# Kernel optimization log

Hardware: AMD Instinct MI355X
Metric: run time of the kernel (lower is better)

Reference implementation:

```python
import jax, jax.numpy as jnp
import numpy as np

B, S, N, C = 8, 256, 256, 64
NH = 8
H, W = 256, 256
D = N * C // NH  # per-head channel dim = 2048
EPS = 1e-12


def window_reverse(windows, ws, Hh, Ww, Cc):
    # windows: (B, S, N, C) -> (B, H*W, C)
    b = windows.shape[0]
    x = windows.reshape(b, Hh // ws[0], Ww // ws[1], ws[0], ws[1], Cc)
    x = x.transpose(0, 1, 3, 2, 4, 5).reshape(b, Hh, Ww, Cc).reshape(b, Hh * Ww, Cc)
    return x


def window_partition(x, ws):
    # x: (B, H, W, C) -> (B, nWin, winElems, C)
    b, hh, ww, cc = x.shape
    x = x.reshape(b, hh // ws[0], ws[0], ww // ws[1], ws[1], cc)
    return x.transpose(0, 1, 3, 2, 4, 5).reshape(b, (hh // ws[0]) * (ww // ws[1]), ws[0] * ws[1], cc)


def setup_inputs() -> dict:
    key = jax.random.key(0)
    ks = jax.random.split(key, 6)
    x = jax.random.normal(ks[0], (B, S, N, C), dtype=jnp.float32)
    qkv_w = jax.random.normal(ks[1], (4 * C, C), dtype=jnp.float32) * 0.02
    qkv_b = jnp.zeros((4 * C,), dtype=jnp.float32)
    proj_w = jax.random.normal(ks[2], (C, C), dtype=jnp.float32) * 0.02
    proj_b = jnp.zeros((C,), dtype=jnp.float32)
    temperature1 = jnp.ones((NH, 1, 1), dtype=jnp.float32)
    temperature2 = jnp.ones((NH, 1, 1), dtype=jnp.float32)
    return {"x": x, "qkv_w": qkv_w, "qkv_b": qkv_b, "proj_w": proj_w,
            "proj_b": proj_b, "temperature1": temperature1, "temperature2": temperature2}


def reference(x, qkv_w, qkv_b, proj_w, proj_b, temperature1, temperature2):
    b, s, n, c = x.shape
    xf = x.reshape(b, s * n, c)
    # fused 4-way qkv projection (q, k, v_H, v_V)
    qkvv = (xf @ qkv_w.T + qkv_b).reshape(b, s, 4, NH, D).transpose(2, 0, 3, 1, 4)
    q, k, v_H, v_V = qkvv[0], qkvv[1], qkvv[2], qkvv[3]  # each (B, NH, S, D)

    # reorient v_V from H-windows (columns) to V-windows (rows)
    v_V = v_V.transpose(0, 2, 1, 3).reshape(b, s, n, c)       # (B,S,N,C)
    v_V = v_V.transpose(0, 2, 1, 3)                           # (B,N,S,C)
    v_V = window_reverse(v_V, (H, 1), H, W, c).reshape(b, H, W, c)
    v_V = window_partition(v_V, (1, W))                       # (B,H,W,C)
    v_V = v_V.transpose(0, 2, 1, 3)                           # (B,W,H,C) == (B,S,N,C)
    v_V = v_V.reshape(b, s, NH, D).transpose(0, 2, 1, 3)      # (B,NH,S,D)

    # cosine attention over S with per-head temperature
    qn = q / jnp.maximum(jnp.linalg.norm(q, axis=-1, keepdims=True), EPS)
    kn = k / jnp.maximum(jnp.linalg.norm(k, axis=-1, keepdims=True), EPS)
    sim = jnp.einsum('bhsd,bhtd->bhst', qn, kn)  # (B,NH,S,S)
    attn_H = jax.nn.softmax(sim * temperature1, axis=-1)
    attn_V = jax.nn.softmax(sim * temperature2, axis=-1)

    x_H = jnp.einsum('bhst,bhtd->bhsd', attn_H, v_H).transpose(0, 2, 1, 3).reshape(b, s * n, c)
    x_V = jnp.einsum('bhst,bhtd->bhsd', attn_V, v_V).transpose(0, 2, 1, 3).reshape(b, s * n, c)

    out = (x_H + x_V) @ proj_w.T + proj_b
    return out.reshape(b, s, n, c)
```

## Files before the change

kernel.cpp:

```cpp
#include <hip/hip_runtime.h>


using half_t = _Float16;
using half8 = __attribute__((ext_vector_type(8))) _Float16;
using f32x4 = __attribute__((ext_vector_type(4))) float;

#define NTOK 524288

#define GLDS(g, l) __builtin_amdgcn_global_load_lds( \
    (const __attribute__((address_space(1))) void*)(g), \
    (__attribute__((address_space(3))) void*)(l), 16, 0, 0)

#define WS_Q      0
#define WS_K      67108864
#define WS_VH     134217728
#define WS_VV     201326592
#define WS_NQ     335544320
#define WS_NK     335609856
#define WS_WH     335675392
#define WS_WP     335708160

__global__ void kW0(const float* __restrict__ qkv_w, const float* __restrict__ proj_w,
                    half_t* __restrict__ Wh, half_t* __restrict__ Wp) {
    int tid = threadIdx.x;
    for (int i = tid; i < 256 * 64; i += 256) Wh[i] = (half_t)qkv_w[i];
    for (int i = tid; i < 64 * 64; i += 256) Wp[i] = (half_t)proj_w[i];
}

__device__ inline void y_tile_mfma(const float* __restrict__ xb,
                                   const half_t* __restrict__ Wh,
                                   int tbase, int hi, int lo,
                                   f32x4 (&acc)[4][4], int wave, int lane) {
    const int l15 = lane & 15, quad = lane >> 4;
#pragma unroll
    for (int kc = 0; kc < 2; ++kc) {
        const int c = kc * 32 + quad * 8;
        half8 afr[4];
#pragma unroll
        for (int mt = 0; mt < 4; ++mt) {
            int m = mt * 16 + l15;
            int token = tbase + (m >> 3) * hi + (m & 7) * lo;
            const float* p = xb + (size_t)token * 64 + c;
            f32x4 f0 = *(const f32x4*)p;
            f32x4 f1 = *(const f32x4*)(p + 4);
            half8 a;
            a[0] = (half_t)f0[0]; a[1] = (half_t)f0[1]; a[2] = (half_t)f0[2]; a[3] = (half_t)f0[3];
            a[4] = (half_t)f1[0]; a[5] = (half_t)f1[1]; a[6] = (half_t)f1[2]; a[7] = (half_t)f1[3];
            afr[mt] = a;
        }
#pragma unroll
        for (int i = 0; i < 4; ++i) {
            int j = (wave * 4 + i) * 16 + l15;
            half8 bfr = *(const half8*)(Wh + j * 64 + c);
#pragma unroll
            for (int mt = 0; mt < 4; ++mt)
                acc[mt][i] = __builtin_amdgcn_mfma_f32_16x16x32_f16(afr[mt], bfr, acc[mt][i], 0, 0, 0);
        }
    }
}

__device__ inline void y_dump_rowmajor(f32x4 (&acc)[4][4], const float* __restrict__ qkv_b,
                                       half_t* ylds, int wave, int lane) {
    const int l15 = lane & 15, quad = lane >> 4;
#pragma unroll
    for (int i = 0; i < 4; ++i) {
        int j = (wave * 4 + i) * 16 + l15;
        float bj = qkv_b[j];
#pragma unroll
        for (int mt = 0; mt < 4; ++mt)
#pragma unroll
            for (int r = 0; r < 4; ++r)
                ylds[(mt * 16 + quad * 4 + r) * 264 + j] = (half_t)(acc[mt][i][r] + bj);
    }
}

__device__ inline void y_dump_transposed(f32x4 (&acc)[4][4], const float* __restrict__ qkv_b,
                                         half_t* yldsT, int wave, int lane) {
    const int l15 = lane & 15, quad = lane >> 4;
#pragma unroll
    for (int i = 0; i < 4; ++i) {
        int j = (wave * 4 + i) * 16 + l15;
        float bj = qkv_b[j];
#pragma unroll
        for (int mt = 0; mt < 4; ++mt)
#pragma unroll
            for (int r = 0; r < 4; ++r)
                yldsT[j * 72 + mt * 16 + quad * 4 + r] = (half_t)(acc[mt][i][r] + bj);
    }
}

__global__ __launch_bounds__(256) void kA1(const float* __restrict__ x,
                                           const half_t* __restrict__ Wh,
                                           const float* __restrict__ qkv_b,
                                           half_t* __restrict__ Q, half_t* __restrict__ K,
                                           float* __restrict__ normQ, float* __restrict__ normK) {
    __shared__ half_t ylds[64 * 264];
    __shared__ float scr[256];
    int idx = blockIdx.x;
    int sb = idx & 31; idx >>= 5;
    int h = idx & 7; idx >>= 3;
    int g = idx & 1; int b = idx >> 1;
    int s0 = sb * 8;
    int n0 = g * 64 + h * 8;
    int tid = threadIdx.x, wave = tid >> 6, lane = tid & 63;
    const float* xb = x + (size_t)b * 65536 * 64;
    f32x4 acc[4][4];
#pragma unroll
    for (int a = 0; a < 4; ++a)
#pragma unroll
        for (int c = 0; c < 4; ++c) acc[a][c] = {0.f, 0.f, 0.f, 0.f};
    y_tile_mfma(xb, Wh, s0 * 256 + n0, 256, 1, acc, wave, lane);
    y_dump_rowmajor(acc, qkv_b, ylds, wave, lane);
    __syncthreads();
    half_t* dst = (g == 0 ? Q : K) + ((size_t)(b * 8 + h) * 256 + s0) * 2048;
    int ns = tid >> 5, jc = (tid & 31) * 8;
#pragma unroll
    for (int si = 0; si < 8; ++si) {
        half8 v = *(const half8*)&ylds[(si * 8 + ns) * 264 + jc];
        *(half8*)(dst + (size_t)si * 2048 + ns * 256 + jc) = v;
    }
    float sum = 0.f;
#pragma unroll
    for (int nn = 0; nn < 8; ++nn) {
        half8 v = *(const half8*)&ylds[((tid >> 5) * 8 + nn) * 264 + (tid & 31) * 8];
#pragma unroll
        for (int e = 0; e < 8; ++e) { float f = (float)v[e]; sum += f * f; }
    }
    scr[tid] = sum;
    __syncthreads();
    if (tid < 8) {
        float s = 0.f;
        for (int k2 = 0; k2 < 32; ++k2) s += scr[tid * 32 + k2];
        float* nd = (g == 0 ? normQ : normK);
        nd[(b * 8 + h) * 256 + s0 + tid] = s;
    }
}

__global__ __launch_bounds__(256) void kA2H(const float* __restrict__ x,
                                            const half_t* __restrict__ Wh,
                                            const float* __restrict__ qkv_b,
                                            half_t* __restrict__ VH) {
    __shared__ half_t yldsT[256 * 72];
    int idx = blockIdx.x;
    int sb = idx & 3; idx >>= 2;
    int nn = idx & 63; int b = idx >> 6;
    int h = nn >> 3, ns = nn & 7;
    int n = 128 + nn;
    int s0 = sb * 64;
    int tid = threadIdx.x, wave = tid >> 6, lane = tid & 63;
    const float* xb = x + (size_t)b * 65536 * 64;
    f32x4 acc[4][4];
#pragma unroll
    for (int a = 0; a < 4; ++a)
#pragma unroll
        for (int c = 0; c < 4; ++c) acc[a][c] = {0.f, 0.f, 0.f, 0.f};
    y_tile_mfma(xb, Wh, s0 * 256 + n, 2048, 256, acc, wave, lane);
    y_dump_transposed(acc, qkv_b, yldsT, wave, lane);
    __syncthreads();
    int jl = lane >> 3, tc = lane & 7;
    half_t* base = VH + ((size_t)(b * 8 + h) * 2048 + ns * 256) * 256 + s0 + tc * 8;
#pragma unroll
    for (int u = 0; u < 8; ++u) {
        int j = wave * 64 + u * 8 + jl;
        half8 v = *(const half8*)&yldsT[j * 72 + tc * 8];
        *(half8*)(base + (size_t)j * 256) = v;
    }
}

__global__ __launch_bounds__(256) void kA2V(const float* __restrict__ x,
                                            const half_t* __restrict__ Wh,
                                            const float* __restrict__ qkv_b,
                                            half_t* __restrict__ VV) {
    __shared__ half_t yldsT[256 * 72];
    int idx = blockIdx.x;
    int st = idx & 255; int b = idx >> 8;
    int h = st >> 5;
    int tid = threadIdx.x, wave = tid >> 6, lane = tid & 63;
    const float* xb = x + (size_t)b * 65536 * 64;
    f32x4 acc[4][4];
#pragma unroll
    for (int a = 0; a < 4; ++a)
#pragma unroll
        for (int c = 0; c < 4; ++c) acc[a][c] = {0.f, 0.f, 0.f, 0.f};
    y_tile_mfma(xb, Wh, st * 256 + 192, 8, 1, acc, wave, lane);
    y_dump_transposed(acc, qkv_b, yldsT, wave, lane);
    __syncthreads();
    int dl = lane >> 3, tc = lane & 7;
    int mbase = wave * 16 + (tc >> 2) * 8 + (tc & 3) * 2;
    half_t* base = VV + ((size_t)(b * 8 + h) * 2048 + (st & 31) * 64) * 256 + wave * 64 + tc * 8;
#pragma unroll
    for (int u = 0; u < 8; ++u) {
        int dm = u * 8 + dl;
        half8 v;
#pragma unroll
        for (int e = 0; e < 8; ++e)
            v[e] = yldsT[((e & 3) * 64 + dm) * 72 + mbase + (e >> 2)];
        *(half8*)(base + (size_t)dm * 256) = v;
    }
}

__global__ __launch_bounds__(1024, 4) void kB(const half_t* __restrict__ Q, const half_t* __restrict__ K,
                                              const half_t* __restrict__ VH, const half_t* __restrict__ VV,
                                              const float* __restrict__ normQ, const float* __restrict__ normK,
                                              const float* __restrict__ temp1, const float* __restrict__ temp2,
                                              const half_t* __restrict__ Wp, const float* __restrict__ proj_b,
                                              float* __restrict__ out) {
    extern __shared__ char smem[];
    char* Ks0 = smem;
    char* Ks1 = smem + 32768;
    char* Qs0 = smem + 65536;
    char* Qs1 = smem + 73728;
    half_t* scratch = (half_t*)smem;
    half_t* PH = (half_t*)(smem + 81920);
    half_t* PV = (half_t*)(smem + 115712);
    float* rq  = (float*)(smem + 149504);
    float* rk  = (float*)(smem + 149760);

    int idx = blockIdx.x;
    int bh = idx & 63;
    int sqb = idx >> 6;
    int h = bh & 7, b = bh >> 3;
    int sq0 = sqb * 64;
    int tid = threadIdx.x, wave = tid >> 6, lane = tid & 63;
    int l15 = lane & 15, quad = lane >> 4;
    float t1 = temp1[h], t2 = temp2[h];
    const half_t* Qb = Q + (size_t)bh * 256 * 2048;
    const half_t* Kb = K + (size_t)bh * 256 * 2048;
    const half_t* VHb = VH + (size_t)bh * 2048 * 256;
    const half_t* VVb = VV + (size_t)bh * 2048 * 256;

    if (tid < 64) rq[tid] = 1.f / fmaxf(sqrtf(normQ[bh * 256 + sq0 + tid]), 1e-12f);
    if (tid < 256) rk[tid] = 1.f / fmaxf(sqrtf(normK[bh * 256 + tid]), 1e-12f);

    {
        const int l7 = lane & 7, l8 = lane >> 3;
        const int swzh = (l7 ^ (l8 & 7)) * 8;
        const half_t* gK0 = Kb + (size_t)(wave * 8 + l8) * 2048 + swzh;
        const half_t* gK1 = Kb + (size_t)(128 + wave * 8 + l8) * 2048 + swzh;
        const half_t* gQ  = Qb + (size_t)(sq0 + (wave & 7) * 8 + l8) * 2048 + swzh;

        auto STAGE = [&](int kk, char* KsB, char* QsB) {
            const int off = kk * 64;
            GLDS(gK0 + off, KsB + wave * 1024);
            GLDS(gK1 + off, KsB + 16384 + wave * 1024);
            if (wave < 8) GLDS(gQ + off, QsB + wave * 1024);
        };

        f32x4 acc1[4];
#pragma unroll
        for (int a = 0; a < 4; ++a) acc1[a] = {0.f, 0.f, 0.f, 0.f};
        const int tcol = wave * 16 + l15;
        const int ts7 = tcol & 7;

        auto COMPUTE = [&](const char* KsB_, const char* QsB_) {
            const half_t* KsB = (const half_t*)KsB_;
            const half_t* QsB = (const half_t*)QsB_;
#pragma unroll
            for (int sub = 0; sub < 2; ++sub) {
                int c16 = sub * 4 + quad;
                half8 bfr = *(const half8*)(KsB + tcol * 64 + (c16 ^ ts7) * 8);
#pragma unroll
                for (int mt = 0; mt < 4; ++mt) {
                    int m = mt * 16 + l15;
                    half8 afr = *(const half8*)(QsB + m * 64 + (c16 ^ (m & 7)) * 8);
                    acc1[mt] = __builtin_amdgcn_mfma_f32_16x16x32_f16(afr, bfr, acc1[mt], 0, 0, 0);
                }
            }
        };

        STAGE(0, Ks0, Qs0);
        __syncthreads();
        for (int kk = 0; kk < 32; kk += 2) {
            if (kk + 1 < 32) STAGE(kk + 1, Ks1, Qs1);
            COMPUTE(Ks0, Qs0);
            __syncthreads();
            if (kk + 2 < 32) STAGE(kk + 2, Ks0, Qs0);
            COMPUTE(Ks1, Qs1);
            __syncthreads();
        }
        float rkt = rk[tcol];
#pragma unroll
        for (int mt = 0; mt < 4; ++mt)
#pragma unroll
            for (int r = 0; r < 4; ++r) {
                int row = mt * 16 + quad * 4 + r;
                PH[row * 264 + tcol] = (half_t)(acc1[mt][r] * rq[row] * rkt);
            }
    }
    __syncthreads();

    {
        int r_ = tid >> 4, cc = tid & 15;
        half_t* phrow = &PH[r_ * 264 + cc * 16];
        half_t* pvrow = &PV[r_ * 264 + cc * 16];
        half8 v0 = *(const half8*)phrow;
        half8 v1 = *(const half8*)(phrow + 8);
        float fv[16];
#pragma unroll
        for (int e = 0; e < 8; ++e) { fv[e] = (float)v0[e]; fv[8 + e] = (float)v1[e]; }
        float mx = fv[0], mn = fv[0];
#pragma unroll
        for (int e = 1; e < 16; ++e) { mx = fmaxf(mx, fv[e]); mn = fminf(mn, fv[e]); }
#pragma unroll
        for (int m = 1; m < 16; m <<= 1) {
            mx = fmaxf(mx, __shfl_xor(mx, m, 16));
            mn = fminf(mn, __shfl_xor(mn, m, 16));
        }
        float mh = (t1 >= 0.f) ? t1 * mx : t1 * mn;
        float mv = (t2 >= 0.f) ? t2 * mx : t2 * mn;
        float sh = 0.f, sv = 0.f;
#pragma unroll
        for (int e = 0; e < 16; ++e) {
            sh += __expf(fv[e] * t1 - mh);
            sv += __expf(fv[e] * t2 - mv);
        }
#pragma unroll
        for (int m = 1; m < 16; m <<= 1) {
            sh += __shfl_xor(sh, m, 16);
            sv += __shfl_xor(sv, m, 16);
        }
        float rh = 1.f / sh, rv = 1.f / sv;
        half8 o0, o1, p0, p1;
#pragma unroll
        for (int e = 0; e < 8; ++e) {
            o0[e] = (half_t)(__expf(fv[e] * t1 - mh) * rh);
            o1[e] = (half_t)(__expf(fv[8 + e] * t1 - mh) * rh);
            p0[e] = (half_t)(__expf(fv[e] * t2 - mv) * rv);
            p1[e] = (half_t)(__expf(fv[8 + e] * t2 - mv) * rv);
        }
        *(half8*)phrow = o0; *(half8*)(phrow + 8) = o1;
        *(half8*)pvrow = p0; *(half8*)(pvrow + 8) = p1;
    }
    __syncthreads();

    half_t* myscr = scratch + wave * 1152;
    float bj[4];
#pragma unroll
    for (int jt = 0; jt < 4; ++jt) bj[jt] = proj_b[jt * 16 + l15];

#pragma unroll
    for (int i2 = 0; i2 < 2; ++i2) {
        int d0 = wave * 64 + i2 * 1024;
        f32x4 acc2[4][4];
#pragma unroll
        for (int a = 0; a < 4; ++a)
#pragma unroll
            for (int c = 0; c < 4; ++c) acc2[a][c] = {0.f, 0.f, 0.f, 0.f};
        for (int kc = 0; kc < 8; ++kc) {
            int tk = kc * 32 + quad * 8;
            half8 afr[4];
#pragma unroll
            for (int mt = 0; mt < 4; ++mt)
                afr[mt] = *(const half8*)&PH[(mt * 16 + l15) * 264 + tk];
#pragma unroll
            for (int nt = 0; nt < 4; ++nt) {
                half8 bfr = *(const half8*)(VHb + (size_t)(d0 + nt * 16 + l15) * 256 + tk);
#pragma unroll
                for (int mt = 0; mt < 4; ++mt)
                    acc2[mt][nt] = __builtin_amdgcn_mfma_f32_16x16x32_f16(afr[mt], bfr, acc2[mt][nt], 0, 0, 0);
            }
#pragma unroll
            for (int mt = 0; mt < 4; ++mt)
                afr[mt] = *(const half8*)&PV[(mt * 16 + l15) * 264 + tk];
#pragma unroll
            for (int nt = 0; nt < 4; ++nt) {
                half8 bfr = *(const half8*)(VVb + (size_t)(d0 + nt * 16 + l15) * 256 + tk);
#pragma unroll
                for (int mt = 0; mt < 4; ++mt)
                    acc2[mt][nt] = __builtin_amdgcn_mfma_f32_16x16x32_f16(afr[mt], bfr, acc2[mt][nt], 0, 0, 0);
            }
        }
        int db = wave + i2 * 16;
#pragma unroll
        for (int mt = 0; mt < 4; ++mt) {
#pragma unroll
            for (int nt = 0; nt < 4; ++nt)
#pragma unroll
                for (int r = 0; r < 4; ++r)
                    myscr[(quad * 4 + r) * 72 + nt * 16 + l15] = (half_t)acc2[mt][nt][r];
            f32x4 accp[4];
#pragma unroll
            for (int jt = 0; jt < 4; ++jt) accp[jt] = {0.f, 0.f, 0.f, 0.f};
#pragma unroll
            for (int kc2 = 0; kc2 < 2; ++kc2) {
                half8 afr = *(const half8*)&myscr[l15 * 72 + kc2 * 32 + quad * 8];
#pragma unroll
                for (int jt = 0; jt < 4; ++jt) {
                    half8 bfr = *(const half8*)(Wp + (jt * 16 + l15) * 64 + kc2 * 32 + quad * 8);
                    accp[jt] = __builtin_amdgcn_mfma_f32_16x16x32_f16(afr, bfr, accp[jt], 0, 0, 0);
                }
            }
#pragma unroll
            for (int jt = 0; jt < 4; ++jt)
#pragma unroll
                for (int r = 0; r < 4; ++r) {
                    int srow = mt * 16 + quad * 4 + r;
                    size_t token = (size_t)b * 65536 + (size_t)(sq0 + srow) * 256 + h * 32 + db;
                    out[token * 64 + jt * 16 + l15] = accp[jt][r] + bj[jt];
                }
        }
    }
}

extern "C" void kernel_launch(void* const* d_in, const int* in_sizes, int n_in,
                              void* d_out, int out_size, void* d_ws, size_t ws_size,
                              hipStream_t stream) {
    const float* x      = (const float*)d_in[0];
    const float* qkv_w  = (const float*)d_in[1];
    const float* qkv_b  = (const float*)d_in[2];
    const float* proj_w = (const float*)d_in[3];
    const float* proj_b = (const float*)d_in[4];
    const float* temp1  = (const float*)d_in[5];
    const float* temp2  = (const float*)d_in[6];
    char* ws = (char*)d_ws;
    half_t* Q   = (half_t*)(ws + WS_Q);
    half_t* K   = (half_t*)(ws + WS_K);
    half_t* VH  = (half_t*)(ws + WS_VH);
    half_t* VV  = (half_t*)(ws + WS_VV);
    float* normQ = (float*)(ws + WS_NQ);
    float* normK = (float*)(ws + WS_NK);
    half_t* Wh  = (half_t*)(ws + WS_WH);
    half_t* Wp  = (half_t*)(ws + WS_WP);
    float* out = (float*)d_out;

    hipFuncSetAttribute((const void*)kB, hipFuncAttributeMaxDynamicSharedMemorySize, 150784);

    kW0<<<1, 256, 0, stream>>>(qkv_w, proj_w, Wh, Wp);
    kA1<<<4096, 256, 0, stream>>>(x, Wh, qkv_b, Q, K, normQ, normK);
    kA2H<<<2048, 256, 0, stream>>>(x, Wh, qkv_b, VH);
    kA2V<<<2048, 256, 0, stream>>>(x, Wh, qkv_b, VV);
    kB<<<256, 1024, 150784, stream>>>(Q, K, VH, VV, normQ, normK, temp1, temp2,
                                      Wp, proj_b, out);
}
```

Baseline: 618.2 us.

## Split output projection out of attention kernel into coalesced separate kernel

The output projection is moved out of the attention kernel kB into a new kernel kC. kB now writes the pre-projection half-precision result to a workspace buffer in a contiguous layout. kC gathers rows per token, runs the 64x64 projection with MFMA, and stores the float output through LDS in coalesced f32x4 writes, replacing kB's scattered scalar stores. The kA2V transposed-store path is also rewritten to scatter into a padded LDS tile and write full 256-wide rows. The cost is an extra 64 MB intermediate round trip and one more kernel launch.

```diff
diff --git a/kernel.cpp b/kernel.cpp
--- a/kernel.cpp
+++ b/kernel.cpp
@@ -15,6 +15,7 @@
 #define WS_K      67108864
 #define WS_VH     134217728
 #define WS_VV     201326592
+#define WS_XHV    268435456
 #define WS_NQ     335544320
 #define WS_NK     335609856
 #define WS_WH     335675392
@@ -171,7 +172,7 @@
                                             const half_t* __restrict__ Wh,
                                             const float* __restrict__ qkv_b,
                                             half_t* __restrict__ VV) {
-    __shared__ half_t yldsT[256 * 72];
+    __shared__ half_t vlds[64 * 264];
     int idx = blockIdx.x;
     int st = idx & 255; int b = idx >> 8;
     int h = st >> 5;
@@ -183,19 +184,32 @@
 #pragma unroll
         for (int c = 0; c < 4; ++c) acc[a][c] = {0.f, 0.f, 0.f, 0.f};
     y_tile_mfma(xb, Wh, st * 256 + 192, 8, 1, acc, wave, lane);
-    y_dump_transposed(acc, qkv_b, yldsT, wave, lane);
-    __syncthreads();
-    int dl = lane >> 3, tc = lane & 7;
-    int mbase = wave * 16 + (tc >> 2) * 8 + (tc & 3) * 2;
-    half_t* base = VV + ((size_t)(b * 8 + h) * 2048 + (st & 31) * 64) * 256 + wave * 64 + tc * 8;
+    {
+        const int l15 = lane & 15, quad = lane >> 4;
+#pragma unroll
+        for (int i = 0; i < 4; ++i) {
+            int j = (wave * 4 + i) * 16 + l15;
+            float bj = qkv_b[j];
+            int dm = j & 63;
+            int jc = j >> 6;
+#pragma unroll
+            for (int mt = 0; mt < 4; ++mt)
+#pragma unroll
+                for (int r = 0; r < 4; ++r) {
+                    int m = mt * 16 + quad * 4 + r;
+                    int t = 32 * (m >> 3) + 4 * (m & 7) + jc;
+                    vlds[dm * 264 + t] = (half_t)(acc[mt][i][r] + bj);
+                }
+        }
+    }
+    __syncthreads();
+    half_t* base = VV + ((size_t)(b * 8 + h) * 2048 + (st & 31) * 64) * 256;
+    int l31 = lane & 31, lh = lane >> 5;
 #pragma unroll
     for (int u = 0; u < 8; ++u) {
-        int dm = u * 8 + dl;
-        half8 v;
-#pragma unroll
-        for (int e = 0; e < 8; ++e)
-            v[e] = yldsT[((e & 3) * 64 + dm) * 72 + mbase + (e >> 2)];
-        *(half8*)(base + (size_t)dm * 256) = v;
+        int dm = u * 8 + wave * 2 + lh;
+        half8 v = *(const half8*)&vlds[dm * 264 + l31 * 8];
+        *(half8*)(base + (size_t)dm * 256 + l31 * 8) = v;
     }
 }
 
@@ -203,14 +217,12 @@
                                               const half_t* __restrict__ VH, const half_t* __restrict__ VV,
                                               const float* __restrict__ normQ, const float* __restrict__ normK,
                                               const float* __restrict__ temp1, const float* __restrict__ temp2,
-                                              const half_t* __restrict__ Wp, const float* __restrict__ proj_b,
-                                              float* __restrict__ out) {
+                                              half_t* __restrict__ xhv) {
     extern __shared__ char smem[];
     char* Ks0 = smem;
     char* Ks1 = smem + 32768;
     char* Qs0 = smem + 65536;
     char* Qs1 = smem + 73728;
-    half_t* scratch = (half_t*)smem;
     half_t* PH = (half_t*)(smem + 81920);
     half_t* PV = (half_t*)(smem + 115712);
     float* rq  = (float*)(smem + 149504);
@@ -333,11 +345,7 @@
     }
     __syncthreads();
 
-    half_t* myscr = scratch + wave * 1152;
-    float bj[4];
-#pragma unroll
-    for (int jt = 0; jt < 4; ++jt) bj[jt] = proj_b[jt * 16 + l15];
-
+    const int rr = lane >> 3, c8 = (lane & 7) * 8;
 #pragma unroll
     for (int i2 = 0; i2 < 2; ++i2) {
         int d0 = wave * 64 + i2 * 1024;
@@ -371,34 +379,62 @@
             }
         }
         int db = wave + i2 * 16;
+        half_t* xbase = xhv + (((size_t)(b * 8 + h) * 32 + db) * 256 + sq0) * 64;
 #pragma unroll
         for (int mt = 0; mt < 4; ++mt) {
+            half_t* myscr = (half_t*)(smem + wave * 5120 + (mt & 1) * 2560);
 #pragma unroll
             for (int nt = 0; nt < 4; ++nt)
 #pragma unroll
                 for (int r = 0; r < 4; ++r)
                     myscr[(quad * 4 + r) * 72 + nt * 16 + l15] = (half_t)acc2[mt][nt][r];
-            f32x4 accp[4];
-#pragma unroll
-            for (int jt = 0; jt < 4; ++jt) accp[jt] = {0.f, 0.f, 0.f, 0.f};
-#pragma unroll
-            for (int kc2 = 0; kc2 < 2; ++kc2) {
-                half8 afr = *(const half8*)&myscr[l15 * 72 + kc2 * 32 + quad * 8];
-#pragma unroll
-                for (int jt = 0; jt < 4; ++jt) {
-                    half8 bfr = *(const half8*)(Wp + (jt * 16 + l15) * 64 + kc2 * 32 + quad * 8);
-                    accp[jt] = __builtin_amdgcn_mfma_f32_16x16x32_f16(afr, bfr, accp[jt], 0, 0, 0);
-                }
+#pragma unroll
+            for (int u = 0; u < 2; ++u) {
+                half8 v = *(const half8*)&myscr[(u * 8 + rr) * 72 + c8];
+                *(half8*)(xbase + (size_t)(mt * 16 + u * 8 + rr) * 64 + c8) = v;
             }
-#pragma unroll
-            for (int jt = 0; jt < 4; ++jt)
-#pragma unroll
-                for (int r = 0; r < 4; ++r) {
-                    int srow = mt * 16 + quad * 4 + r;
-                    size_t token = (size_t)b * 65536 + (size_t)(sq0 + srow) * 256 + h * 32 + db;
-                    out[token * 64 + jt * 16 + l15] = accp[jt][r] + bj[jt];
-                }
-        }
+        }
+    }
+}
+
+__global__ __launch_bounds__(256) void kC(const half_t* __restrict__ xhv, const half_t* __restrict__ Wp,
+                                          const float* __restrict__ proj_b, float* __restrict__ out) {
+    __shared__ float ot[64 * 68];
+    int tid = threadIdx.x, wave = tid >> 6, lane = tid & 63;
+    int l15 = lane & 15, quad = lane >> 4;
+    size_t T0 = (size_t)blockIdx.x * 64;
+    int b = (int)(T0 >> 16);
+    int s = (int)((T0 >> 8) & 255);
+    int n0 = (int)(T0 & 255);
+    f32x4 acc[4];
+#pragma unroll
+    for (int a = 0; a < 4; ++a) acc[a] = {0.f, 0.f, 0.f, 0.f};
+#pragma unroll
+    for (int kc = 0; kc < 2; ++kc) {
+        int c = kc * 32 + quad * 8;
+        half8 bfr = *(const half8*)(Wp + (wave * 16 + l15) * 64 + c);
+#pragma unroll
+        for (int mt = 0; mt < 4; ++mt) {
+            int n = n0 + mt * 16 + l15;
+            int hh = n >> 5, db = n & 31;
+            const half_t* arow = xhv + (((size_t)(b * 8 + hh) * 32 + db) * 256 + s) * 64;
+            half8 afr = *(const half8*)(arow + c);
+            acc[mt] = __builtin_amdgcn_mfma_f32_16x16x32_f16(afr, bfr, acc[mt], 0, 0, 0);
+        }
+    }
+    float bj = proj_b[wave * 16 + l15];
+#pragma unroll
+    for (int mt = 0; mt < 4; ++mt)
+#pragma unroll
+        for (int r = 0; r < 4; ++r)
+            ot[(mt * 16 + quad * 4 + r) * 68 + wave * 16 + l15] = acc[mt][r] + bj;
+    __syncthreads();
+    int row = tid >> 2;
+#pragma unroll
+    for (int u = 0; u < 4; ++u) {
+        int col = (tid & 3) * 4 + u * 16;
+        f32x4 v = *(const f32x4*)&ot[row * 68 + col];
+        *(f32x4*)(out + (T0 + row) * 64 + col) = v;
     }
 }
 
@@ -417,6 +453,7 @@
     half_t* K   = (half_t*)(ws + WS_K);
     half_t* VH  = (half_t*)(ws + WS_VH);
     half_t* VV  = (half_t*)(ws + WS_VV);
+    half_t* xhv = (half_t*)(ws + WS_XHV);
     float* normQ = (float*)(ws + WS_NQ);
     float* normK = (float*)(ws + WS_NK);
     half_t* Wh  = (half_t*)(ws + WS_WH);
@@ -429,6 +466,6 @@
     kA1<<<4096, 256, 0, stream>>>(x, Wh, qkv_b, Q, K, normQ, normK);
     kA2H<<<2048, 256, 0, stream>>>(x, Wh, qkv_b, VH);
     kA2V<<<2048, 256, 0, stream>>>(x, Wh, qkv_b, VV);
-    kB<<<256, 1024, 150784, stream>>>(Q, K, VH, VV, normQ, normK, temp1, temp2,
-                                      Wp, proj_b, out);
-}
+    kB<<<256, 1024, 150784, stream>>>(Q, K, VH, VV, normQ, normK, temp1, temp2, xhv);
+    kC<<<8192, 256, 0, stream>>>(xhv, Wp, proj_b, out);
+}
```

Result: faster. 590.8 us (-4.4%).
